# Optimization experiments

Measured on AMD Instinct MI355X. Metric: run time of the kernel, lower is better.

## Reference

```python
import jax, jax.numpy as jnp
import numpy as np

D_K = 128.0  # temp_softmax buffer value


def setup_inputs() -> dict:
    key = jax.random.key(0)
    kq, kk, kv = jax.random.split(key, 3)
    B, S, D = 16, 2048, 128
    q = jax.random.normal(kq, (B, S, D), dtype=jnp.float32)
    k = jax.random.normal(kk, (B, S, D), dtype=jnp.float32)
    v = jax.random.normal(kv, (B, S, D), dtype=jnp.float32)
    mask = jnp.zeros((S, S), dtype=jnp.float32)  # additive mask: 0 = keep, -inf = masked
    return {"q": q, "k": k, "v": v, "mask": mask}


def reference(q, k, v, mask):
    # scores: [B, Sq, Sk]
    attn = jnp.einsum('bqd,bkd->bqk', q, k)
    attn = attn / jnp.sqrt(jnp.asarray(D_K, dtype=attn.dtype))  # scale=True
    attn = attn + mask  # broadcast [Sq,Sk] over batch
    attn = jax.nn.softmax(attn, axis=2)
    # dropout=None -> no dropout
    output = jnp.einsum('bqk,bkd->bqd', attn, v)
    return (output, attn)
```

## Files before the change

### kernel.cpp

```cpp
#include <hip/hip_runtime.h>

#define BATCH 16
#define SEQ   2048
#define DH    128
#define BM    64
#define BN    64
#define NT    (SEQ / BN)

typedef float  f32x4 __attribute__((ext_vector_type(4)));
typedef short  s16x8 __attribute__((ext_vector_type(8)));
typedef short  s16x4 __attribute__((ext_vector_type(4)));
typedef unsigned short u16;

__device__ __forceinline__ short f2bf(float f) {
    union { float f; unsigned u; } a; a.f = f;
    unsigned r = a.u + 0x7FFFu + ((a.u >> 16) & 1u);
    return (short)(r >> 16);
}

__device__ __forceinline__ void gl_lds16(const void* g, void* l) {
    __builtin_amdgcn_global_load_lds(
        (const __attribute__((address_space(1))) void*)g,
        (__attribute__((address_space(3))) void*)l, 16, 0, 0);
}

__global__ __launch_bounds__(256)
void conv_qk(const float* __restrict__ q, const float* __restrict__ k,
             const float* __restrict__ mask, u16* __restrict__ qw,
             char* __restrict__ kw, int* __restrict__ flag) {
    size_t e = ((size_t)blockIdx.x * 256 + threadIdx.x) * 8;

    f32x4 f0 = *(const f32x4*)(q + e);
    f32x4 f1 = *(const f32x4*)(q + e + 4);
    s16x8 w;
    w[0]=f2bf(f0[0]); w[1]=f2bf(f0[1]); w[2]=f2bf(f0[2]); w[3]=f2bf(f0[3]);
    w[4]=f2bf(f1[0]); w[5]=f2bf(f1[1]); w[6]=f2bf(f1[2]); w[7]=f2bf(f1[3]);
    *(s16x8*)(qw + e) = w;

    f0 = *(const f32x4*)(k + e);
    f1 = *(const f32x4*)(k + e + 4);
    w[0]=f2bf(f0[0]); w[1]=f2bf(f0[1]); w[2]=f2bf(f0[2]); w[3]=f2bf(f0[3]);
    w[4]=f2bf(f1[0]); w[5]=f2bf(f1[1]); w[6]=f2bf(f1[2]); w[7]=f2bf(f1[3]);
    int    d0   = (int)(e & 127);
    size_t srow = e >> 7;
    int    row  = (int)(srow & 63);
    size_t tile = srow >> 6;
    *(s16x8*)(kw + (tile << 14) +
              ((((row << 8) + (d0 << 1)) ^ ((row & 7) << 4)))) = w;

    f0 = *(const f32x4*)(mask + e);
    f1 = *(const f32x4*)(mask + e + 4);
    bool nz = f0[0]!=0.f || f0[1]!=0.f || f0[2]!=0.f || f0[3]!=0.f ||
              f1[0]!=0.f || f1[1]!=0.f || f1[2]!=0.f || f1[3]!=0.f;
    if (__ballot(nz) != 0ull) {
        if ((threadIdx.x & 63) == 0) atomicOr(flag, 1);
    }
}

__global__ __launch_bounds__(256)
void conv_v(const float* __restrict__ v, char* __restrict__ vw) {
    __shared__ u16 lt[64][132];
    const int tid = threadIdx.x;
    const int kt = blockIdx.x, b = blockIdx.y;
    const float* src = v + (((size_t)b * SEQ + kt * 64) << 7);
    #pragma unroll
    for (int i = 0; i < 8; ++i) {
        int c = i * 256 + tid;
        int j = c >> 5, d0 = (c & 31) * 4;
        f32x4 f = *(const f32x4*)(src + (j << 7) + d0);
        s16x4 w4; w4[0]=f2bf(f[0]); w4[1]=f2bf(f[1]); w4[2]=f2bf(f[2]); w4[3]=f2bf(f[3]);
        *(s16x4*)&lt[j][d0] = w4;
    }
    __syncthreads();
    char* dstt = vw + (((size_t)b * NT + kt) << 14);
    #pragma unroll
    for (int i = 0; i < 4; ++i) {
        int c = i * 256 + tid;
        int d = c >> 3, jg = c & 7;
        s16x8 w8;
        #pragma unroll
        for (int s = 0; s < 8; ++s) w8[s] = (short)lt[jg * 8 + s][d];
        *(s16x8*)(dstt + (((d << 7) + jg * 16) ^ ((d & 7) << 4))) = w8;
    }
}

#define KOFF0 0
#define VOFF0 32768
#define POFF  65536

#define STAGE16K(SRC, LOFF) do {                                   \
    const char* _s = (SRC); const int _o = tid * 16;               \
    gl_lds16(_s + _o,         smem + (LOFF) + _o);                 \
    gl_lds16(_s + _o + 4096,  smem + (LOFF) + _o + 4096);          \
    gl_lds16(_s + _o + 8192,  smem + (LOFF) + _o + 8192);          \
    gl_lds16(_s + _o + 12288, smem + (LOFF) + _o + 12288);         \
} while (0)

__global__ __launch_bounds__(256, 2)
void attn_main(const u16* __restrict__ qw, const char* __restrict__ kw,
               const char* __restrict__ vw, const float* __restrict__ mask,
               const int* __restrict__ flag,
               float* __restrict__ out_o, float* __restrict__ out_p) {
    extern __shared__ char smem[];
    const int tid  = threadIdx.x;
    const int wave = tid >> 6, lane = tid & 63, quad = lane >> 4, l16 = lane & 15;
    const int b = blockIdx.y, q0 = blockIdx.x * BM;
    const float CS  = 0.08838834764831845f * 1.4426950408889634f;
    const float L2E = 1.4426950408889634f;
    const int hm = *flag;
    const int sw = (l16 & 7) << 4;

    const u16* qp = qw + (((size_t)b * SEQ + (size_t)(q0 + wave * 16 + l16)) << 7);
    s16x8 aq[4];
    #pragma unroll
    for (int s = 0; s < 4; ++s)
        aq[s] = *(const s16x8*)(qp + s * 32 + quad * 8);

    size_t moff[4], prow[4];
    #pragma unroll
    for (int r = 0; r < 4; ++r) {
        int row = q0 + wave * 16 + quad * 4 + r;
        moff[r] = (size_t)row * SEQ;
        prow[r] = ((size_t)b * SEQ + row) * SEQ;
    }

    const char* kb = kw + ((size_t)(b * NT) << 14);
    const char* vb = vw + ((size_t)(b * NT) << 14);

    float msk[4][4] = {{0,0,0,0},{0,0,0,0},{0,0,0,0},{0,0,0,0}};
    float lsum[4] = {0.f, 0.f, 0.f, 0.f};

    STAGE16K(kb, KOFF0);
    __syncthreads();
    int kof = KOFF0;
    for (int kt = 0; kt < NT; ++kt) {
        if (kt + 1 < NT) STAGE16K(kb + ((size_t)(kt + 1) << 14), kof ^ 16384);
        const int j0 = kt * BN;
        if (hm) {
            #pragma unroll
            for (int t = 0; t < 4; ++t)
                #pragma unroll
                for (int r = 0; r < 4; ++r)
                    msk[t][r] = mask[moff[r] + j0 + t * 16 + l16] * L2E;
        }
        #pragma unroll
        for (int t = 0; t < 4; ++t) {
            f32x4 c = {0.f, 0.f, 0.f, 0.f};
            #pragma unroll
            for (int s = 0; s < 4; ++s) {
                const s16x8 bk = *(const s16x8*)(smem + kof +
                    (((((t * 16 + l16) << 8) + s * 64 + quad * 16)) ^ sw));
                c = __builtin_amdgcn_mfma_f32_16x16x32_bf16(aq[s], bk, c, 0, 0, 0);
            }
            #pragma unroll
            for (int r = 0; r < 4; ++r)
                lsum[r] += exp2f(c[r] * CS + msk[t][r]);
        }
        __syncthreads();
        kof ^= 16384;
    }

    float linv[4];
    #pragma unroll
    for (int r = 0; r < 4; ++r) {
        float s = lsum[r];
        s += __shfl_xor(s, 1);
        s += __shfl_xor(s, 2);
        s += __shfl_xor(s, 4);
        s += __shfl_xor(s, 8);
        linv[r] = 1.0f / s;
    }

    f32x4 acc[8];
    #pragma unroll
    for (int n = 0; n < 8; ++n) acc[n] = (f32x4){0.f, 0.f, 0.f, 0.f};

    STAGE16K(kb, KOFF0);
    STAGE16K(vb, VOFF0);
    __syncthreads();
    int bof = 0;
    for (int kt = 0; kt < NT; ++kt) {
        if (kt + 1 < NT) {
            STAGE16K(kb + ((size_t)(kt + 1) << 14), KOFF0 + (bof ^ 16384));
            STAGE16K(vb + ((size_t)(kt + 1) << 14), VOFF0 + (bof ^ 16384));
        }
        const int j0 = kt * BN;
        if (hm) {
            #pragma unroll
            for (int t = 0; t < 4; ++t)
                #pragma unroll
                for (int r = 0; r < 4; ++r)
                    msk[t][r] = mask[moff[r] + j0 + t * 16 + l16] * L2E;
        }
        const int kbase = KOFF0 + bof;
        const int vbase = VOFF0 + bof;

        #pragma unroll
        for (int t = 0; t < 4; ++t) {
            f32x4 c = {0.f, 0.f, 0.f, 0.f};
            #pragma unroll
            for (int s = 0; s < 4; ++s) {
                const s16x8 bk = *(const s16x8*)(smem + kbase +
                    (((((t * 16 + l16) << 8) + s * 64 + quad * 16)) ^ sw));
                c = __builtin_amdgcn_mfma_f32_16x16x32_bf16(aq[s], bk, c, 0, 0, 0);
            }
            #pragma unroll
            for (int r = 0; r < 4; ++r) {
                float p = exp2f(c[r] * CS + msk[t][r]) * linv[r];
                out_p[prow[r] + j0 + t * 16 + l16] = p;
                const int pr = wave * 16 + quad * 4 + r;
                *(short*)(smem + POFF +
                    ((((pr << 7) + ((t * 16 + l16) << 1))) ^ ((pr & 7) << 4))) = f2bf(p);
            }
        }
        #pragma unroll
        for (int s2 = 0; s2 < 2; ++s2) {
            const int par = wave * 16 + l16;
            const s16x8 pa = *(const s16x8*)(smem + POFF +
                ((((par << 7) + s2 * 64 + quad * 16)) ^ sw));
            #pragma unroll
            for (int n = 0; n < 8; ++n) {
                const s16x8 bv = *(const s16x8*)(smem + vbase +
                    (((((n * 16 + l16) << 7) + s2 * 64 + quad * 16)) ^ sw));
                acc[n] = __builtin_amdgcn_mfma_f32_16x16x32_bf16(pa, bv, acc[n], 0, 0, 0);
            }
        }
        __syncthreads();
        bof ^= 16384;
    }

    #pragma unroll
    for (int n = 0; n < 8; ++n) {
        #pragma unroll
        for (int r = 0; r < 4; ++r) {
            int row = q0 + wave * 16 + quad * 4 + r;
            out_o[((size_t)b * SEQ + row) * DH + n * 16 + l16] = acc[n][r];
        }
    }
}

extern "C" void kernel_launch(void* const* d_in, const int* in_sizes, int n_in,
                              void* d_out, int out_size, void* d_ws, size_t ws_size,
                              hipStream_t stream) {
    (void)in_sizes; (void)n_in; (void)out_size; (void)ws_size;
    const float* q    = (const float*)d_in[0];
    const float* k    = (const float*)d_in[1];
    const float* v    = (const float*)d_in[2];
    const float* mask = (const float*)d_in[3];
    float* out_o = (float*)d_out;
    float* out_p = out_o + (size_t)BATCH * SEQ * DH;

    char* ws   = (char*)d_ws;
    u16*  qw   = (u16*)ws;
    char* kw   = ws + ((size_t)8 << 20);
    char* vw   = ws + ((size_t)16 << 20);
    int*  flag = (int*)(ws + ((size_t)24 << 20));

    hipMemsetAsync(flag, 0, 4, stream);
    conv_qk<<<dim3(2048), dim3(256), 0, stream>>>(q, k, mask, qw, kw, flag);
    conv_v<<<dim3(NT, BATCH), dim3(256), 0, stream>>>(v, vw);

    static bool attr_done = false;
    if (!attr_done) {
        (void)hipFuncSetAttribute((const void*)attn_main,
                                  hipFuncAttributeMaxDynamicSharedMemorySize, 73728);
        attr_done = true;
    }
    attn_main<<<dim3(SEQ / BM, BATCH), dim3(256), 73728, stream>>>(
        qw, kw, vw, mask, flag, out_o, out_p);
}
```

Measured before the change: 420.9 us.

## Split work across waves by key column and output dim instead of query rows

Each wave now holds Q fragments for all 64 query rows and computes a 16-key-column slice of the score tile, so each K fragment is read from LDS once per wave instead of four times. Row sums are combined across waves through shared memory. The PV product is split by output dimension, with each wave owning 32 of the 128 columns. A barrier is placed between writing P to LDS and reading it, because P now crosses waves. Stores of the probabilities and the output are made nontemporal. The change costs extra registers for the Q fragments (64 VGPRs) and extra barriers, which may hurt occupancy at 2 blocks per SIMD.

Measured after the change: 399.1 us. 1.05x faster.

```diff
diff --git a/kernel.cpp b/kernel.cpp
--- a/kernel.cpp
+++ b/kernel.cpp
@@ -108,27 +108,26 @@
     const float CS  = 0.08838834764831845f * 1.4426950408889634f;
     const float L2E = 1.4426950408889634f;
     const int hm = *flag;
-    const int sw = (l16 & 7) << 4;
-
-    const u16* qp = qw + (((size_t)b * SEQ + (size_t)(q0 + wave * 16 + l16)) << 7);
-    s16x8 aq[4];
-    #pragma unroll
-    for (int s = 0; s < 4; ++s)
-        aq[s] = *(const s16x8*)(qp + s * 32 + quad * 8);
-
-    size_t moff[4], prow[4];
-    #pragma unroll
-    for (int r = 0; r < 4; ++r) {
-        int row = q0 + wave * 16 + quad * 4 + r;
-        moff[r] = (size_t)row * SEQ;
-        prow[r] = ((size_t)b * SEQ + row) * SEQ;
+    const int sw   = (l16 & 7) << 4;
+    const int kcol = wave * 16 + l16;
+
+    s16x8 aq[4][4];
+    #pragma unroll
+    for (int mt = 0; mt < 4; ++mt) {
+        const u16* qp = qw + ((size_t)(b * SEQ + q0 + mt * 16 + l16) << 7);
+        #pragma unroll
+        for (int s = 0; s < 4; ++s)
+            aq[mt][s] = *(const s16x8*)(qp + s * 32 + quad * 8);
     }
 
     const char* kb = kw + ((size_t)(b * NT) << 14);
     const char* vb = vw + ((size_t)(b * NT) << 14);
 
-    float msk[4][4] = {{0,0,0,0},{0,0,0,0},{0,0,0,0},{0,0,0,0}};
-    float lsum[4] = {0.f, 0.f, 0.f, 0.f};
+    float lsum[4][4];
+    #pragma unroll
+    for (int mt = 0; mt < 4; ++mt)
+        #pragma unroll
+        for (int r = 0; r < 4; ++r) lsum[mt][r] = 0.f;
 
     STAGE16K(kb, KOFF0);
     __syncthreads();
@@ -136,44 +135,66 @@
     for (int kt = 0; kt < NT; ++kt) {
         if (kt + 1 < NT) STAGE16K(kb + ((size_t)(kt + 1) << 14), kof ^ 16384);
         const int j0 = kt * BN;
-        if (hm) {
-            #pragma unroll
-            for (int t = 0; t < 4; ++t)
+        s16x8 bk[4];
+        #pragma unroll
+        for (int s = 0; s < 4; ++s)
+            bk[s] = *(const s16x8*)(smem + kof +
+                (((kcol << 8) + s * 64 + quad * 16) ^ sw));
+        #pragma unroll
+        for (int mt = 0; mt < 4; ++mt) {
+            f32x4 c = {0.f, 0.f, 0.f, 0.f};
+            #pragma unroll
+            for (int s = 0; s < 4; ++s)
+                c = __builtin_amdgcn_mfma_f32_16x16x32_bf16(aq[mt][s], bk[s], c, 0, 0, 0);
+            float mk[4] = {0.f, 0.f, 0.f, 0.f};
+            if (hm) {
                 #pragma unroll
                 for (int r = 0; r < 4; ++r)
-                    msk[t][r] = mask[moff[r] + j0 + t * 16 + l16] * L2E;
-        }
-        #pragma unroll
-        for (int t = 0; t < 4; ++t) {
-            f32x4 c = {0.f, 0.f, 0.f, 0.f};
-            #pragma unroll
-            for (int s = 0; s < 4; ++s) {
-                const s16x8 bk = *(const s16x8*)(smem + kof +
-                    (((((t * 16 + l16) << 8) + s * 64 + quad * 16)) ^ sw));
-                c = __builtin_amdgcn_mfma_f32_16x16x32_bf16(aq[s], bk, c, 0, 0, 0);
+                    mk[r] = mask[(size_t)(q0 + mt * 16 + quad * 4 + r) * SEQ + j0 + kcol] * L2E;
             }
             #pragma unroll
             for (int r = 0; r < 4; ++r)
-                lsum[r] += exp2f(c[r] * CS + msk[t][r]);
+                lsum[mt][r] += exp2f(c[r] * CS + mk[r]);
         }
         __syncthreads();
         kof ^= 16384;
     }
 
-    float linv[4];
-    #pragma unroll
-    for (int r = 0; r < 4; ++r) {
-        float s = lsum[r];
-        s += __shfl_xor(s, 1);
-        s += __shfl_xor(s, 2);
-        s += __shfl_xor(s, 4);
-        s += __shfl_xor(s, 8);
-        linv[r] = 1.0f / s;
-    }
-
-    f32x4 acc[8];
-    #pragma unroll
-    for (int n = 0; n < 8; ++n) acc[n] = (f32x4){0.f, 0.f, 0.f, 0.f};
+    float* ls = (float*)(smem + POFF);
+    #pragma unroll
+    for (int mt = 0; mt < 4; ++mt)
+        #pragma unroll
+        for (int r = 0; r < 4; ++r) {
+            float s = lsum[mt][r];
+            s += __shfl_xor(s, 1);
+            s += __shfl_xor(s, 2);
+            s += __shfl_xor(s, 4);
+            s += __shfl_xor(s, 8);
+            lsum[mt][r] = s;
+        }
+    if (l16 == 0) {
+        #pragma unroll
+        for (int mt = 0; mt < 4; ++mt)
+            #pragma unroll
+            for (int r = 0; r < 4; ++r)
+                ls[(mt * 16 + quad * 4 + r) * 4 + wave] = lsum[mt][r];
+    }
+    __syncthreads();
+    float linv[4][4];
+    #pragma unroll
+    for (int mt = 0; mt < 4; ++mt)
+        #pragma unroll
+        for (int r = 0; r < 4; ++r) {
+            f32x4 t = *(const f32x4*)&ls[(mt * 16 + quad * 4 + r) * 4];
+            linv[mt][r] = 1.0f / (t[0] + t[1] + t[2] + t[3]);
+        }
+
+    f32x4 acc[4][2];
+    #pragma unroll
+    for (int amt = 0; amt < 4; ++amt) {
+        acc[amt][0] = (f32x4){0.f, 0.f, 0.f, 0.f};
+        acc[amt][1] = (f32x4){0.f, 0.f, 0.f, 0.f};
+    }
 
     STAGE16K(kb, KOFF0);
     STAGE16K(vb, VOFF0);
@@ -185,44 +206,50 @@
             STAGE16K(vb + ((size_t)(kt + 1) << 14), VOFF0 + (bof ^ 16384));
         }
         const int j0 = kt * BN;
-        if (hm) {
-            #pragma unroll
-            for (int t = 0; t < 4; ++t)
+        s16x8 bk[4];
+        #pragma unroll
+        for (int s = 0; s < 4; ++s)
+            bk[s] = *(const s16x8*)(smem + KOFF0 + bof +
+                (((kcol << 8) + s * 64 + quad * 16) ^ sw));
+        #pragma unroll
+        for (int mt = 0; mt < 4; ++mt) {
+            f32x4 c = {0.f, 0.f, 0.f, 0.f};
+            #pragma unroll
+            for (int s = 0; s < 4; ++s)
+                c = __builtin_amdgcn_mfma_f32_16x16x32_bf16(aq[mt][s], bk[s], c, 0, 0, 0);
+            float mk[4] = {0.f, 0.f, 0.f, 0.f};
+            if (hm) {
                 #pragma unroll
                 for (int r = 0; r < 4; ++r)
-                    msk[t][r] = mask[moff[r] + j0 + t * 16 + l16] * L2E;
-        }
-        const int kbase = KOFF0 + bof;
+                    mk[r] = mask[(size_t)(q0 + mt * 16 + quad * 4 + r) * SEQ + j0 + kcol] * L2E;
+            }
+            #pragma unroll
+            for (int r = 0; r < 4; ++r) {
+                float p = exp2f(c[r] * CS + mk[r]) * linv[mt][r];
+                __builtin_nontemporal_store(p,
+                    &out_p[((size_t)(b * SEQ + q0 + mt * 16 + quad * 4 + r) << 11) + j0 + kcol]);
+                const int pr = mt * 16 + quad * 4 + r;
+                *(short*)(smem + POFF +
+                    (((pr << 7) + (kcol << 1)) ^ ((pr & 7) << 4))) = f2bf(p);
+            }
+        }
+        __builtin_amdgcn_sched_barrier(0);
+        asm volatile("s_waitcnt lgkmcnt(0)\n\ts_barrier" ::: "memory");
+        __builtin_amdgcn_sched_barrier(0);
+
         const int vbase = VOFF0 + bof;
-
-        #pragma unroll
-        for (int t = 0; t < 4; ++t) {
-            f32x4 c = {0.f, 0.f, 0.f, 0.f};
-            #pragma unroll
-            for (int s = 0; s < 4; ++s) {
-                const s16x8 bk = *(const s16x8*)(smem + kbase +
-                    (((((t * 16 + l16) << 8) + s * 64 + quad * 16)) ^ sw));
-                c = __builtin_amdgcn_mfma_f32_16x16x32_bf16(aq[s], bk, c, 0, 0, 0);
-            }
-            #pragma unroll
-            for (int r = 0; r < 4; ++r) {
-                float p = exp2f(c[r] * CS + msk[t][r]) * linv[r];
-                out_p[prow[r] + j0 + t * 16 + l16] = p;
-                const int pr = wave * 16 + quad * 4 + r;
-                *(short*)(smem + POFF +
-                    ((((pr << 7) + ((t * 16 + l16) << 1))) ^ ((pr & 7) << 4))) = f2bf(p);
-            }
-        }
         #pragma unroll
         for (int s2 = 0; s2 < 2; ++s2) {
-            const int par = wave * 16 + l16;
-            const s16x8 pa = *(const s16x8*)(smem + POFF +
-                ((((par << 7) + s2 * 64 + quad * 16)) ^ sw));
-            #pragma unroll
-            for (int n = 0; n < 8; ++n) {
-                const s16x8 bv = *(const s16x8*)(smem + vbase +
-                    (((((n * 16 + l16) << 7) + s2 * 64 + quad * 16)) ^ sw));
-                acc[n] = __builtin_amdgcn_mfma_f32_16x16x32_bf16(pa, bv, acc[n], 0, 0, 0);
+            const s16x8 bv0 = *(const s16x8*)(smem + vbase +
+                ((((wave * 32 + l16) << 7) + s2 * 64 + quad * 16) ^ sw));
+            const s16x8 bv1 = *(const s16x8*)(smem + vbase +
+                ((((wave * 32 + 16 + l16) << 7) + s2 * 64 + quad * 16) ^ sw));
+            #pragma unroll
+            for (int amt = 0; amt < 4; ++amt) {
+                const s16x8 pa = *(const s16x8*)(smem + POFF +
+                    ((((amt * 16 + l16) << 7) + s2 * 64 + quad * 16) ^ sw));
+                acc[amt][0] = __builtin_amdgcn_mfma_f32_16x16x32_bf16(pa, bv0, acc[amt][0], 0, 0, 0);
+                acc[amt][1] = __builtin_amdgcn_mfma_f32_16x16x32_bf16(pa, bv1, acc[amt][1], 0, 0, 0);
             }
         }
         __syncthreads();
@@ -230,13 +257,14 @@
     }
 
     #pragma unroll
-    for (int n = 0; n < 8; ++n) {
-        #pragma unroll
-        for (int r = 0; r < 4; ++r) {
-            int row = q0 + wave * 16 + quad * 4 + r;
-            out_o[((size_t)b * SEQ + row) * DH + n * 16 + l16] = acc[n][r];
-        }
-    }
+    for (int amt = 0; amt < 4; ++amt)
+        #pragma unroll
+        for (int nt = 0; nt < 2; ++nt)
+            #pragma unroll
+            for (int r = 0; r < 4; ++r)
+                __builtin_nontemporal_store(acc[amt][nt][r],
+                    &out_o[((size_t)(b * SEQ + q0 + amt * 16 + quad * 4 + r) << 7)
+                           + wave * 32 + nt * 16 + l16]);
 }
 
 extern "C" void kernel_launch(void* const* d_in, const int* in_sizes, int n_in,
```
